# Optimization experiments

Measured on AMD Instinct MI355X. Metric: run time of the kernel, lower is better.

Reference implementation:

```python
import jax, jax.numpy as jnp
import numpy as np

BS, SEQ, D_IN, D_OUT = 4, 1024, 1024, 1024
N_SKILLS, RANK = 8, 4
SCALING = 1.0  # lora_alpha / rank, folded into one constant
NEG_INF = -1e38


def setup_inputs() -> dict:
    key = jax.random.key(0)
    ks = jax.random.split(key, 5)
    x = jax.random.normal(ks[0], (BS, SEQ, D_IN), jnp.float32)
    phi = jax.random.normal(ks[1], (D_IN, N_SKILLS), jnp.float32) * 0.02
    lora_a = jax.random.normal(ks[2], (N_SKILLS, D_IN, RANK), jnp.float32) * 0.02
    lora_b = jax.random.normal(ks[3], (N_SKILLS, RANK, D_OUT), jnp.float32) * 0.02
    W = jax.random.normal(ks[4], (D_OUT, D_IN), jnp.float32) * 0.02
    b = jnp.zeros((D_OUT,), jnp.float32)
    # left-padded sequences with an instruction prefix right after the padding
    pad_len = np.array([100, 0, 250, 50])
    inst_len = 300
    pad = np.zeros((BS, SEQ), np.int32)
    inst = np.zeros((BS, SEQ), np.int32)
    for i in range(BS):
        pad[i, pad_len[i]:] = 1
        inst[i, pad_len[i]:pad_len[i] + inst_len] = 1
    return {"x": x, "phi": phi, "lora_a": lora_a, "lora_b": lora_b,
            "W": W, "b": b,
            "inst_mask": jnp.asarray(inst), "pad_mask": jnp.asarray(pad)}


def _causal_prefix_mask(inst_mask, pad_mask):
    # faithful port of create_causal_prefix_mask (padding_side='left')
    bs, seq = inst_mask.shape
    first_one = jnp.argmax(inst_mask, axis=1, keepdims=True)          # [b,1]
    n_ones = jnp.sum(inst_mask, axis=1, keepdims=True)                # [b,1]
    thresh = first_one + n_ones                                       # last_one_idx + 1
    exp = jnp.broadcast_to(thresh, (bs, seq))                         # [b,s]
    inv = jnp.maximum(seq - exp - jnp.arange(seq)[None, :], 0)[:, ::-1]
    m = (exp + inv) * pad_mask                                        # [b,s]
    m3 = m[:, :, None] * pad_mask[:, None, :]                         # [b,s,s]
    ar = jnp.arange(seq)[None, None, :]
    return ar < m3                                                    # bool [b,s,s]


def reference(x, phi, lora_a, lora_b, W, b, inst_mask, pad_mask):
    # router: mixing logits per token per skill
    mw = jnp.einsum('bsd,dn->bsn', x, phi)                            # [b,s,k]
    cm = _causal_prefix_mask(inst_mask, pad_mask)                     # [b,s,s]
    padf = pad_mask.astype(x.dtype)
    # expand over attended positions p, mask, softmax over p
    logits = jnp.where(cm[..., None], mw[:, :, None, :], NEG_INF)     # [b,s,p,k]
    logits = jnp.transpose(logits, (0, 3, 1, 2))                      # [b,k,s,p]
    D = jax.nn.softmax(logits, axis=-1)
    D = D * padf[:, None, :, None]                                    # zero padded query rows
    # token mixing: contract over source tokens (last axis of D)
    input_mixed = jnp.einsum('bsd,bkps->bkpd', x, D)                  # [b,k,s,d]
    # per-skill LoRA (n_splits == 1, q squeezed)
    ar_r = jnp.einsum('bksd,kdr->bskr', input_mixed, lora_a)          # [b,s,k,r]
    ad = jnp.einsum('bskr,krd->bskd', ar_r, lora_b)                   # [b,s,k,d_out]
    # softmax-weighted combine over skills
    C = jax.nn.softmax(mw, axis=-1)
    adapter_out = jnp.einsum('bsk,bskd->bsd', C, ad) * SCALING
    base = jnp.einsum('bsd,od->bso', x, W) + b
    return base + adapter_out
```

## Files before the change

kernel.cpp:

```cpp
#include <hip/hip_runtime.h>
#include <hip/hip_bf16.h>
#include <cstdint>

#define SEQ   1024
#define DOUT  1024
#define KDIM  1024
#define MTOT  4096

typedef __bf16 bf16x8 __attribute__((ext_vector_type(8)));
typedef float  f32x4  __attribute__((ext_vector_type(4)));

__device__ inline unsigned short f2bf(float f) {
  union { float f; unsigned u; } a; a.f = f;
  unsigned r = a.u + 0x7fff + ((a.u >> 16) & 1);
  return (unsigned short)(r >> 16);
}

__device__ inline void gl16(const void* g, void* l) {
  __builtin_amdgcn_global_load_lds((__attribute__((address_space(1))) void*)g,
                                   (__attribute__((address_space(3))) void*)l, 16, 0, 0);
}

__global__ __launch_bounds__(256) void k_prep(const float4* __restrict__ x, ushort4* __restrict__ xb,
                                              const float* __restrict__ phi, const float* __restrict__ la,
                                              unsigned short* __restrict__ Wc) {
  int blk = blockIdx.x, tid = threadIdx.x;
  if (blk < 4096) {
    int i = blk * 256 + tid;
    float4 v = x[i];
    ushort4 o; o.x = f2bf(v.x); o.y = f2bf(v.y); o.z = f2bf(v.z); o.w = f2bf(v.w);
    xb[i] = o;
  } else {
    int i = (blk - 4096) * 256 + tid;
    int row = 1024 + (i >> 10), d = i & 1023;
    float v;
    if (row < 1032)       v = phi[d * 8 + (row - 1024)];
    else if (row < 1064)  { int kr = row - 1032; v = la[(kr >> 2) * 4096 + d * 4 + (kr & 3)]; }
    else                  v = 0.f;
    Wc[(size_t)row * 1024 + d] = f2bf(v);
  }
}

__global__ __launch_bounds__(256) void k_mwz(const unsigned short* __restrict__ xb,
                                             const unsigned short* __restrict__ Wc0,
                                             const float* __restrict__ W, const float* __restrict__ lb,
                                             const int* __restrict__ inst,
                                             unsigned short* __restrict__ Wc, unsigned short* __restrict__ B2T,
                                             int* __restrict__ thr, float* __restrict__ mwzP) {
  __shared__ unsigned short As[64 * 32];
  __shared__ unsigned short Bs[48 * 32];
  int blk = blockIdx.x, t = threadIdx.x;
  if (blk >= 256) {
    if (blk < 4352) {
      size_t i = (size_t)(blk - 256) * 256 + t;
      Wc[i] = f2bf(W[i]);
    } else if (blk < 4480) {
      int i = (blk - 4352) * 256 + t;
      int n = i >> 5, kr = i & 31;
      B2T[i] = f2bf(lb[kr * 1024 + n]);
    } else {
      int b = t >> 6, lane = t & 63;
      int fo = 1 << 30, no = 0;
#pragma unroll
      for (int j = 0; j < 16; ++j) {
        int p = j * 64 + lane;
        int iv = inst[b * SEQ + p];
        if (iv > 0) fo = min(fo, p);
        no += iv;
      }
#pragma unroll
      for (int d = 1; d < 64; d <<= 1) { fo = min(fo, __shfl_xor(fo, d)); no += __shfl_xor(no, d); }
      if (lane == 0) thr[b] = (no > 0) ? fo + no : 0;
    }
    return;
  }
  int bm = blk & 63, ks = blk >> 6;
  int wave = t >> 6, lane = t & 63;
  int quad = lane >> 4, lr = lane & 15;
  f32x4 acc[3];
#pragma unroll
  for (int i = 0; i < 3; ++i) acc[i] = (f32x4){0.f, 0.f, 0.f, 0.f};
  const unsigned short* aG = xb + (size_t)bm * 64 * KDIM + ks * 256;
  const unsigned short* bG = Wc0 + (size_t)1024 * KDIM + ks * 256;
  int r0 = t >> 2, c0 = (t & 3) * 8;
  for (int kb = 0; kb < 256; kb += 32) {
    __syncthreads();
    gl16(aG + (size_t)r0 * KDIM + kb + c0, &As[wave * 512]);
    if (t < 192) gl16(bG + (size_t)r0 * KDIM + kb + c0, &Bs[wave * 512]);
    __syncthreads();
    bf16x8 af = *(const bf16x8*)&As[(wave * 16 + lr) * 32 + quad * 8];
#pragma unroll
    for (int ni = 0; ni < 3; ++ni) {
      bf16x8 bfr = *(const bf16x8*)&Bs[(ni * 16 + lr) * 32 + quad * 8];
      acc[ni] = __builtin_amdgcn_mfma_f32_16x16x32_bf16(af, bfr, acc[ni], 0, 0, 0);
    }
  }
#pragma unroll
  for (int ni = 0; ni < 3; ++ni) {
    int c = ni * 16 + lr;
#pragma unroll
    for (int rg = 0; rg < 4; ++rg) {
      int row = bm * 64 + wave * 16 + quad * 4 + rg;
      if (c < 40) mwzP[(size_t)(ks * 40 + c) * MTOT + row] = acc[ni][rg];
    }
  }
}

__global__ __launch_bounds__(1024) void k_scan_gate(const float* __restrict__ mwzP,
                                                    const int* __restrict__ pad, const int* __restrict__ thr,
                                                    unsigned short* __restrict__ gb) {
  int b = blockIdx.x, c = blockIdx.y;
  int tid = threadIdx.x, wv = tid >> 6, lane = tid & 63;
  __shared__ float wsz[16], wsp[16];
  __shared__ float sv, spc;
  int q = b * SEQ + tid;
  float pm = (float)pad[q];
  float z = 0.f;
#pragma unroll
  for (int s = 0; s < 4; ++s) z += mwzP[(size_t)(s * 40 + 8 + c) * MTOT + q];
  z *= pm;
  float vz = z, vp = pm;
#pragma unroll
  for (int d = 1; d < 64; d <<= 1) {
    float oz = __shfl_up(vz, d), op = __shfl_up(vp, d);
    if (lane >= d) { vz += oz; vp += op; }
  }
  if (lane == 63) { wsz[wv] = vz; wsp[wv] = vp; }
  __syncthreads();
  if (wv == 0 && lane < 16) {
    float oz = wsz[lane], op = wsp[lane], sz = oz, sp = op;
#pragma unroll
    for (int d = 1; d < 16; d <<= 1) {
      float tz = __shfl_up(sz, d), tp = __shfl_up(sp, d);
      if (lane >= d) { sz += tz; sp += tp; }
    }
    wsz[lane] = sz - oz; wsp[lane] = sp - op;
  }
  __syncthreads();
  vz += wsz[wv]; vp += wsp[wv];
  int th = thr[b];
  if (th > 0 && tid == th - 1) { sv = vz; spc = vp; }
  __syncthreads();
  unsigned short o = 0;
  if (pm != 0.f) {
    bool own = (tid + 1 >= th);
    float Tv  = own ? vz : sv;
    float cnt = own ? vp : spc;
    float C[8], mx = -1e30f;
#pragma unroll
    for (int k = 0; k < 8; ++k) {
      float m = 0.f;
#pragma unroll
      for (int s = 0; s < 4; ++s) m += mwzP[(size_t)(s * 40 + k) * MTOT + q];
      C[k] = m; mx = fmaxf(mx, m);
    }
    float sm = 0.f;
#pragma unroll
    for (int k = 0; k < 8; ++k) { C[k] = __expf(C[k] - mx); sm += C[k]; }
    o = f2bf(C[c >> 2] * Tv / (sm * cnt));
  }
  gb[(size_t)q * 32 + c] = o;
}

__global__ __launch_bounds__(256) void k_gemm(const unsigned short* __restrict__ A,
                                              const unsigned short* __restrict__ Wc,
                                              const unsigned short* __restrict__ gb,
                                              const unsigned short* __restrict__ B2T,
                                              float* __restrict__ out,
                                              const float* __restrict__ bias) {
  __shared__ unsigned short As[128 * 32];
  __shared__ unsigned short Bs[64 * 32];
  int bm = blockIdx.x, bn = blockIdx.y;
  int t = threadIdx.x;
  int wave = t >> 6, lane = t & 63;
  int wr = wave >> 1, wc = wave & 1;
  int quad = lane >> 4, lr = lane & 15;
  f32x4 acc[4][2];
#pragma unroll
  for (int i = 0; i < 4; i++)
#pragma unroll
    for (int j = 0; j < 2; j++) acc[i][j] = (f32x4){0.f, 0.f, 0.f, 0.f};

  {
    bf16x8 ga[4], gBf[2];
#pragma unroll
    for (int mi = 0; mi < 4; mi++)
      ga[mi] = *(const bf16x8*)(gb + (size_t)(bm * 128 + wr * 64 + mi * 16 + lr) * 32 + quad * 8);
#pragma unroll
    for (int ni = 0; ni < 2; ni++)
      gBf[ni] = *(const bf16x8*)(B2T + (size_t)(bn * 64 + wc * 32 + ni * 16 + lr) * 32 + quad * 8);
#pragma unroll
    for (int mi = 0; mi < 4; mi++)
#pragma unroll
      for (int ni = 0; ni < 2; ni++)
        acc[mi][ni] = __builtin_amdgcn_mfma_f32_16x16x32_bf16(ga[mi], gBf[ni], acc[mi][ni], 0, 0, 0);
  }

  const unsigned short* aG = A + (size_t)bm * 128 * KDIM;
  const unsigned short* bG = Wc + (size_t)bn * 64 * KDIM;
  int r0 = t >> 2, c0 = (t & 3) * 8;

  for (int kb = 0; kb < KDIM; kb += 32) {
    __syncthreads();
    gl16(aG + (size_t)r0 * KDIM + kb + c0,        &As[wave * 512]);
    gl16(aG + (size_t)(r0 + 64) * KDIM + kb + c0, &As[2048 + wave * 512]);
    gl16(bG + (size_t)r0 * KDIM + kb + c0,        &Bs[wave * 512]);
    __syncthreads();
    bf16x8 af[4], bfr[2];
#pragma unroll
    for (int mi = 0; mi < 4; mi++) af[mi]  = *(const bf16x8*)&As[(wr * 64 + mi * 16 + lr) * 32 + quad * 8];
#pragma unroll
    for (int ni = 0; ni < 2; ni++) bfr[ni] = *(const bf16x8*)&Bs[(wc * 32 + ni * 16 + lr) * 32 + quad * 8];
#pragma unroll
    for (int mi = 0; mi < 4; mi++)
#pragma unroll
      for (int ni = 0; ni < 2; ni++)
        acc[mi][ni] = __builtin_amdgcn_mfma_f32_16x16x32_bf16(af[mi], bfr[ni], acc[mi][ni], 0, 0, 0);
  }

#pragma unroll
  for (int mi = 0; mi < 4; mi++) {
#pragma unroll
    for (int ni = 0; ni < 2; ni++) {
      int col = bn * 64 + wc * 32 + ni * 16 + lr;
      float bv = bias[col];
#pragma unroll
      for (int rg = 0; rg < 4; ++rg) {
        int row = bm * 128 + wr * 64 + mi * 16 + quad * 4 + rg;
        out[(size_t)row * DOUT + col] = acc[mi][ni][rg] + bv;
      }
    }
  }
}

extern "C" void kernel_launch(void* const* d_in, const int* in_sizes, int n_in,
                              void* d_out, int out_size, void* d_ws, size_t ws_size,
                              hipStream_t stream) {
  const float* x    = (const float*)d_in[0];
  const float* phi  = (const float*)d_in[1];
  const float* la   = (const float*)d_in[2];
  const float* lb   = (const float*)d_in[3];
  const float* W    = (const float*)d_in[4];
  const float* bias = (const float*)d_in[5];
  const int*   inst = (const int*)d_in[6];
  const int*   pad  = (const int*)d_in[7];
  float* out = (float*)d_out;

  char* ws = (char*)d_ws;
  unsigned short* xb  = (unsigned short*)ws;
  unsigned short* Wc  = (unsigned short*)(ws + 8388608);
  unsigned short* B2T = (unsigned short*)(ws + 10584064);
  float* mwzP = (float*)(ws + 10649600);
  unsigned short* gb  = (unsigned short*)(ws + 13271040);
  int*   thr  = (int*)(ws + 13533184);

  hipLaunchKernelGGL(k_prep,      dim3(4288),   dim3(256),  0, stream,
                     (const float4*)x, (ushort4*)xb, phi, la, Wc);
  hipLaunchKernelGGL(k_mwz,       dim3(4481),   dim3(256),  0, stream,
                     xb, Wc, W, lb, inst, Wc, B2T, thr, mwzP);
  hipLaunchKernelGGL(k_scan_gate, dim3(4, 32),  dim3(1024), 0, stream, mwzP, pad, thr, gb);
  hipLaunchKernelGGL(k_gemm,      dim3(32, 16), dim3(256),  0, stream, xb, Wc, gb, B2T, out, bias);
}
```

Baseline: 113.5 us.

## Double-buffer GEMM LDS tiles with K=64 and XOR-swizzled layout

The main GEMM loop moves from a single-buffered 32-wide K tile with two barriers per step to double-buffered 64-wide K tiles. The next tile's global-to-LDS loads are issued before the current tile's MFMAs run, leaving one barrier per iteration. Columns are XOR-swizzled by row to reduce LDS bank conflicts on the fragment reads. LDS use grows about fourfold, which may lower occupancy, and the correctness of the async loads relies on the trailing barrier.

```diff
diff --git a/kernel.cpp b/kernel.cpp
--- a/kernel.cpp
+++ b/kernel.cpp
@@ -168,8 +168,8 @@
                                               const unsigned short* __restrict__ B2T,
                                               float* __restrict__ out,
                                               const float* __restrict__ bias) {
-  __shared__ unsigned short As[128 * 32];
-  __shared__ unsigned short Bs[64 * 32];
+  __shared__ __align__(16) unsigned short As[2][128 * 64];
+  __shared__ __align__(16) unsigned short Bs[2][64 * 64];
   int bm = blockIdx.x, bn = blockIdx.y;
   int t = threadIdx.x;
   int wave = t >> 6, lane = t & 63;
@@ -198,24 +198,51 @@
 
   const unsigned short* aG = A + (size_t)bm * 128 * KDIM;
   const unsigned short* bG = Wc + (size_t)bn * 64 * KDIM;
-  int r0 = t >> 2, c0 = (t & 3) * 8;
-
-  for (int kb = 0; kb < KDIM; kb += 32) {
+
+  auto stage = [&](int b, int kb) {
+#pragma unroll
+    for (int i = 0; i < 4; ++i) {
+      int g = i * 256 + t;
+      int r = g >> 3, c = (g & 7) * 8;
+      int cs = c ^ ((r & 7) * 8);
+      gl16(aG + (size_t)r * KDIM + kb + cs, &As[b][i * 2048 + wave * 512]);
+    }
+#pragma unroll
+    for (int i = 0; i < 2; ++i) {
+      int g = i * 256 + t;
+      int r = g >> 3, c = (g & 7) * 8;
+      int cs = c ^ ((r & 7) * 8);
+      gl16(bG + (size_t)r * KDIM + kb + cs, &Bs[b][i * 2048 + wave * 512]);
+    }
+  };
+
+  stage(0, 0);
+  __syncthreads();
+  for (int it = 0; it < 16; ++it) {
+    int cur = it & 1;
+    if (it < 15) stage(cur ^ 1, (it + 1) * 64);
+#pragma unroll
+    for (int kk = 0; kk < 2; ++kk) {
+      bf16x8 af[4], bfr[2];
+#pragma unroll
+      for (int mi = 0; mi < 4; mi++) {
+        int R = wr * 64 + mi * 16 + lr;
+        int cc = (kk * 32 + quad * 8) ^ ((R & 7) * 8);
+        af[mi] = *(const bf16x8*)&As[cur][R * 64 + cc];
+      }
+#pragma unroll
+      for (int ni = 0; ni < 2; ni++) {
+        int R = wc * 32 + ni * 16 + lr;
+        int cc = (kk * 32 + quad * 8) ^ ((R & 7) * 8);
+        bfr[ni] = *(const bf16x8*)&Bs[cur][R * 64 + cc];
+      }
+#pragma unroll
+      for (int mi = 0; mi < 4; mi++)
+#pragma unroll
+        for (int ni = 0; ni < 2; ni++)
+          acc[mi][ni] = __builtin_amdgcn_mfma_f32_16x16x32_bf16(af[mi], bfr[ni], acc[mi][ni], 0, 0, 0);
+    }
     __syncthreads();
-    gl16(aG + (size_t)r0 * KDIM + kb + c0,        &As[wave * 512]);
-    gl16(aG + (size_t)(r0 + 64) * KDIM + kb + c0, &As[2048 + wave * 512]);
-    gl16(bG + (size_t)r0 * KDIM + kb + c0,        &Bs[wave * 512]);
-    __syncthreads();
-    bf16x8 af[4], bfr[2];
-#pragma unroll
-    for (int mi = 0; mi < 4; mi++) af[mi]  = *(const bf16x8*)&As[(wr * 64 + mi * 16 + lr) * 32 + quad * 8];
-#pragma unroll
-    for (int ni = 0; ni < 2; ni++) bfr[ni] = *(const bf16x8*)&Bs[(wc * 32 + ni * 16 + lr) * 32 + quad * 8];
-#pragma unroll
-    for (int mi = 0; mi < 4; mi++)
-#pragma unroll
-      for (int ni = 0; ni < 2; ni++)
-        acc[mi][ni] = __builtin_amdgcn_mfma_f32_16x16x32_bf16(af[mi], bfr[ni], acc[mi][ni], 0, 0, 0);
   }
 
 #pragma unroll
```

New measurement: 111.2 us. 2.0% less time.
